# Performance work log

Measured on AMD Instinct MI355X. Metric: run time of the kernel, lower is better.

The kernel has to match this reference:

```python
import jax, jax.numpy as jnp
import numpy as np

B, S = 64, 200
DK = 32           # d_k = d_a = d_e
NQ = 4096         # n_question
NE = 20000        # n_exercise
NAT = 2000
NIT = 2000


def _xavier(k, shape):
    a = float(np.sqrt(6.0 / (shape[0] + shape[1])))
    return jax.random.uniform(k, shape, jnp.float32, -a, a)


def setup_inputs() -> dict:
    key = jax.random.key(0)
    ks = jax.random.split(key, 24)
    d = {}
    d['e_data'] = jax.random.randint(ks[0], (B, S), 0, NE)
    d['at_data'] = jax.random.randint(ks[1], (B, S), 0, NAT)
    d['it_data'] = jax.random.randint(ks[2], (B, S), 0, NIT)
    d['a_data'] = jax.random.randint(ks[3], (B, S), 0, 2).astype(jnp.float32)
    # binary Q-matrix: ~64 skills per exercise on average
    d['q_matrix'] = (jax.random.uniform(ks[4], (NE + 10, NQ + 1)) < (64.0 / NQ)).astype(jnp.float32)
    d['E_e'] = _xavier(ks[5], (NE + 10, DK))
    d['E_at'] = _xavier(ks[6], (NAT + 10, DK))
    d['E_it'] = _xavier(ks[7], (NIT + 10, DK))
    d['W1'] = _xavier(ks[8], (DK, 3 * DK)); d['b1'] = jnp.zeros((DK,), jnp.float32)
    d['W2'] = _xavier(ks[9], (DK, 4 * DK)); d['b2'] = jnp.zeros((DK,), jnp.float32)
    d['W3'] = _xavier(ks[10], (DK, 4 * DK)); d['b3'] = jnp.zeros((DK,), jnp.float32)
    d['W4'] = _xavier(ks[11], (DK, 3 * DK)); d['b4'] = jnp.zeros((DK,), jnp.float32)
    d['W5'] = _xavier(ks[12], (DK, 2 * DK)); d['b5'] = jnp.zeros((DK,), jnp.float32)
    d['h0'] = _xavier(ks[13], (NQ + 1, DK))
    return d


def _forward(e_data, at_data, it_data, a_data, q_matrix, E_e, E_at, E_it,
             W1, b1, W2, b2, W3, b3, W4, b4, W5, b5, h0):
    e_emb = E_e[e_data]                    # [B,S,DK]
    at_emb = E_at[at_data]                 # [B,S,DK]
    it_emb = E_it[it_data]                 # [B,S,DK]
    a_rep = jnp.broadcast_to(a_data[:, :, None], (B, S, DK))  # repeat answer to d_a
    all_learning = jnp.einsum('bsf,kf->bsk', jnp.concatenate([e_emb, at_emb, a_rep], -1), W1) + b1

    h_pre0 = jnp.broadcast_to(h0[None], (B, NQ + 1, DK))
    h_tilde0 = jnp.einsum('bn,bnd->bd', q_matrix[e_data[:, 0]], h_pre0)
    W4h, W4l, W4i = W4[:, :DK], W4[:, DK:2 * DK], W4[:, 2 * DK:]

    def step(carry, xs):
        learning_pre, h_pre, h_tilde_pre = carry
        e_t, it, learning, e_next_emb, e_next = xs
        q_e = q_matrix[e_t]                               # [B,NQ+1] gather
        x = jnp.concatenate([learning_pre, it, learning, h_tilde_pre], -1)  # [B,4DK]
        lg = jnp.tanh(x @ W2.T + b2)
        gl = jax.nn.sigmoid(x @ W3.T + b3)
        LG = gl * (lg + 1.0) * 0.5                        # [B,DK]
        LG_tilde = q_e[:, :, None] * LG[:, None, :]       # scatter (outer product), dropout off (eval)
        gamma_f = jax.nn.sigmoid(h_pre @ W4h.T + (LG @ W4l.T + it @ W4i.T + b4)[:, None, :])
        h = LG_tilde + gamma_f * h_pre                    # [B,NQ+1,DK]
        h_tilde = jnp.einsum('bn,bnd->bd', q_matrix[e_next], h)
        y = jax.nn.sigmoid(jnp.concatenate([e_next_emb, h_tilde], -1) @ W5.T + b5).sum(-1) / DK
        return (learning, h, h_tilde), y

    xs = (e_data[:, :-1].T,
          jnp.swapaxes(it_emb[:, :-1], 0, 1),
          jnp.swapaxes(all_learning[:, :-1], 0, 1),
          jnp.swapaxes(e_emb[:, 1:], 0, 1),
          e_data[:, 1:].T)
    init = (jnp.zeros((B, DK), jnp.float32), h_pre0, h_tilde0)
    _, ys = jax.lax.scan(step, init, xs)                  # ys: [S-1,B]
    pred = jnp.concatenate([jnp.zeros((B, 1), jnp.float32), ys.T], axis=1)
    return pred


def reference(e_data, at_data, it_data, a_data, q_matrix, E_e, E_at, E_it,
              W1, b1, W2, b2, W3, b3, W4, b4, W5, b5, h0):
    return _forward(e_data, at_data, it_data, a_data, q_matrix, E_e, E_at, E_it,
                    W1, b1, W2, b2, W3, b3, W4, b4, W5, b5, h0)
```

## Files before the change

### kernel.cpp

```cpp
#include <hip/hip_runtime.h>

#define Bv    64
#define Sv    200
#define DKv   32
#define NQ1v  4097
#define NWG   8
#define TPB   256
#define ROWS  2
#define NSTEP 199

typedef unsigned long long u64;

__device__ __forceinline__ float fsig(float x) {
  return __builtin_amdgcn_rcpf(1.0f + __builtin_amdgcn_exp2f(x * -1.4426950408889634f));
}
__device__ __forceinline__ float ftanh_(float x) {
  return fmaf(2.0f, fsig(2.0f * x), -1.0f);
}
__device__ __forceinline__ u64 packvt(float v, unsigned tag) {
  return ((u64)tag << 32) | (u64)__float_as_uint(v);
}
__device__ __forceinline__ u64 fresh_read(u64* p) {
  return __hip_atomic_fetch_add(p, 0ull, __ATOMIC_RELAXED, __HIP_MEMORY_SCOPE_AGENT);
}
__device__ __forceinline__ void fresh_write(u64* p, u64 v) {
  (void)__hip_atomic_exchange(p, v, __ATOMIC_RELAXED, __HIP_MEMORY_SCOPE_AGENT);
}

__global__ void lpkt_init(float* out) {
  int i = threadIdx.x;
  if (i < Bv) out[i * Sv] = 0.0f;
}

__global__ __launch_bounds__(TPB, 2) void lpkt_main(
    const int* __restrict__ e_data, const int* __restrict__ at_data,
    const int* __restrict__ it_data, const float* __restrict__ a_data,
    const float* __restrict__ q_matrix,
    const float* __restrict__ E_e, const float* __restrict__ E_at, const float* __restrict__ E_it,
    const float* __restrict__ W1, const float* __restrict__ b1,
    const float* __restrict__ W2, const float* __restrict__ b2,
    const float* __restrict__ W3, const float* __restrict__ b3,
    const float* __restrict__ W4, const float* __restrict__ b4,
    const float* __restrict__ W5, const float* __restrict__ b5,
    const float* __restrict__ h0, float* __restrict__ out,
    u64* __restrict__ partial)
{
  const int tid = threadIdx.x;
  const int wg  = blockIdx.x & (NWG - 1);
  const int b   = blockIdx.x / NWG;
  const int k   = tid & 31;
  const int p   = tid >> 5;
  const int nbase = wg * (TPB * ROWS);

  __shared__ float W23T[128 * 64];
  __shared__ __align__(16) float W1L[32 * 100];
  __shared__ __align__(16) float W4L[32 * 100];
  __shared__ __align__(16) float W5L[32 * 68];
  __shared__ float bL[5 * 32];
  __shared__ __align__(16) float xw_lds[96];
  __shared__ __align__(16) float it_lds[DKv];
  __shared__ __align__(16) float lcA[DKv], lcB[DKv];
  __shared__ __align__(16) float ht_lds[DKv];
  __shared__ __align__(16) float LG_lds[DKv];
  __shared__ __align__(16) float c_lds[DKv];
  __shared__ __align__(16) float red[8][DKv];
  __shared__ __align__(16) float red2[8][DKv];
  __shared__ float ht_part[DKv];
  __shared__ __align__(16) float h49[DKv];

  for (int idx = tid; idx < 128 * 32; idx += TPB) {
    int j = idx & 127, kk = idx >> 7;
    W23T[j * 64 + 2 * kk]     = W2[kk * 128 + j];
    W23T[j * 64 + 2 * kk + 1] = W3[kk * 128 + j];
  }
  for (int idx = tid; idx < 32 * 96; idx += TPB) {
    int r = idx / 96, c = idx % 96;
    W1L[r * 100 + c] = W1[idx];
    W4L[r * 100 + c] = W4[idx];
  }
  for (int idx = tid; idx < 32 * 64; idx += TPB) {
    int r = idx >> 6, c = idx & 63;
    W5L[r * 68 + c] = W5[idx];
  }
  if (tid < 32) {
    bL[0 * 32 + tid] = b1[tid]; bL[1 * 32 + tid] = b2[tid];
    bL[2 * 32 + tid] = b3[tid]; bL[3 * 32 + tid] = b4[tid];
    bL[4 * 32 + tid] = b5[tid];
  }
  if (tid < DKv) { ht_part[tid] = 0.0f; lcB[tid] = 0.0f; }
  if (wg == 0 && tid < DKv) h49[tid] = h0[4096 * DKv + tid];

  float h[ROWS][DKv];
#pragma unroll
  for (int r = 0; r < ROWS; r++) {
    const float4* hp = (const float4*)(h0 + (size_t)(nbase + r * TPB + tid) * DKv);
#pragma unroll
    for (int i = 0; i < 8; i++) {
      float4 v = hp[i];
      h[r][4*i] = v.x; h[r][4*i+1] = v.y; h[r][4*i+2] = v.z; h[r][4*i+3] = v.w;
    }
  }
  const int e0 = e_data[b * Sv];
  const float* q0 = q_matrix + (size_t)e0 * NQ1v;
  float qc[ROWS];
#pragma unroll
  for (int r = 0; r < ROWS; r++) qc[r] = q0[nbase + r * TPB + tid];
  float qc49 = (wg == 0 && tid < DKv) ? q0[4096] : 0.0f;
  __syncthreads();

#pragma unroll
  for (int r = 0; r < ROWS; r++) {
    if (qc[r] != 0.0f) {
#pragma unroll
      for (int kk = 0; kk < DKv; kk++) atomicAdd(&ht_part[kk], h[r][kk]);
    }
  }
  if (wg == 0 && tid < DKv && qc49 != 0.0f) atomicAdd(&ht_part[tid], h49[tid]);
  __syncthreads();
  if (tid < DKv)
    fresh_write(&partial[((size_t)(1 % 3) * Bv + b) * (NWG * DKv) + wg * DKv + tid],
                packvt(ht_part[tid], 1u));

  for (int t = 0; t < NSTEP; t++) {
    float* lc_cur  = (t & 1) ? lcB : lcA;
    float* lc_prev = (t & 1) ? lcA : lcB;
    const unsigned tau_g = (unsigned)(t + 1);
    const unsigned tau_p = (unsigned)(t + 2);

    const int ecur  = e_data[b * Sv + t];
    const int enext = e_data[b * Sv + t + 1];
    const int atc   = at_data[b * Sv + t];
    const int itc   = it_data[b * Sv + t];
    const float av  = a_data[b * Sv + t];
    const float* qnr = q_matrix + (size_t)enext * NQ1v;
    float qn[ROWS];
#pragma unroll
    for (int r = 0; r < ROWS; r++) qn[r] = qnr[nbase + r * TPB + tid];
    float qn49 = (wg == 0 && tid < DKv) ? qnr[4096] : 0.0f;

    if (tid < 96)
      xw_lds[tid] = (tid < 32) ? E_e[(size_t)ecur * DKv + tid]
                  : (tid < 64) ? E_at[(size_t)atc * DKv + (tid - 32)] : av;
    else if (tid < 128)
      it_lds[tid - 96] = E_it[(size_t)itc * DKv + (tid - 96)];

    float acc[ROWS][DKv];
#pragma unroll
    for (int kk = 0; kk < DKv; kk++) {
      float a0 = 0.0f, a1 = 0.0f;
#pragma unroll
      for (int d = 0; d < DKv; d += 4) {
        float4 w = *(const float4*)&W4[kk * 96 + d];
        a0 = fmaf(w.x, h[0][d+0], a0); a1 = fmaf(w.x, h[1][d+0], a1);
        a0 = fmaf(w.y, h[0][d+1], a0); a1 = fmaf(w.y, h[1][d+1], a1);
        a0 = fmaf(w.z, h[0][d+2], a0); a1 = fmaf(w.z, h[1][d+2], a1);
        a0 = fmaf(w.w, h[0][d+3], a0); a1 = fmaf(w.w, h[1][d+3], a1);
      }
      acc[0][kk] = a0; acc[1][kk] = a1;
    }
    __syncthreads();

    if (tid < DKv) {
      u64* pb = partial + ((size_t)(tau_g % 3) * Bv + b) * (NWG * DKv) + tid;
      u64 v[NWG];
      for (;;) {
        bool ok = true;
#pragma unroll
        for (int w2 = 0; w2 < NWG; w2++) {
          v[w2] = fresh_read(&pb[w2 * DKv]);
          ok = ok && ((unsigned)(v[w2] >> 32) == tau_g);
        }
        if (ok) break;
        __builtin_amdgcn_s_sleep(2);
      }
      float s = 0.0f;
#pragma unroll
      for (int w2 = 0; w2 < NWG; w2++) s += __uint_as_float((unsigned)v[w2]);
      ht_lds[tid] = s;
    } else if (tid >= 64 && tid < 96) {
      const int kx = tid - 64;
      float s = bL[0 * 32 + kx];
      const float4* wp = (const float4*)&W1L[kx * 100];
      const float4* xp = (const float4*)xw_lds;
#pragma unroll
      for (int i = 0; i < 24; i++) {
        float4 w = wp[i]; float4 x = xp[i];
        s = fmaf(x.x, w.x, s); s = fmaf(x.y, w.y, s);
        s = fmaf(x.z, w.z, s); s = fmaf(x.w, w.w, s);
      }
      lc_cur[kx] = s;
    }
    __syncthreads();

    {
      const int seg = p >> 1;
      const float* sp = (seg == 0) ? lc_prev : (seg == 1) ? it_lds
                      : (seg == 2) ? lc_cur  : ht_lds;
      const int off = (p & 1) * 16;
      float xv[16];
#pragma unroll
      for (int i = 0; i < 4; i++) {
        float4 v = ((const float4*)(sp + off))[i];
        xv[4*i] = v.x; xv[4*i+1] = v.y; xv[4*i+2] = v.z; xv[4*i+3] = v.w;
      }
      float s2 = 0.0f, s3 = 0.0f;
      const int jb = 16 * p;
#pragma unroll
      for (int i = 0; i < 16; i++) {
        float2 w = *(const float2*)&W23T[(jb + i) * 64 + 2 * k];
        s2 = fmaf(xv[i], w.x, s2);
        s3 = fmaf(xv[i], w.y, s3);
      }
      red[p][k] = s2; red2[p][k] = s3;
    }
    __syncthreads();

    if (tid < DKv) {
      float s2 = bL[1 * 32 + tid], s3 = bL[2 * 32 + tid];
#pragma unroll
      for (int pp = 0; pp < 8; pp++) { s2 += red[pp][tid]; s3 += red2[pp][tid]; }
      LG_lds[tid] = fsig(s3) * (ftanh_(s2) + 1.0f) * 0.5f;
    } else if (tid >= 128 && tid < 160) ht_part[tid - 128] = 0.0f;
    __syncthreads();

    {
      const float* up = (p < 4) ? (LG_lds + 8 * p) : (it_lds + 8 * (p - 4));
      const float4* wp = (const float4*)&W4L[k * 100 + 32 + 8 * p];
      float4 w0 = wp[0], w1 = wp[1];
      float pc = 0.0f;
      pc = fmaf(up[0], w0.x, pc); pc = fmaf(up[1], w0.y, pc);
      pc = fmaf(up[2], w0.z, pc); pc = fmaf(up[3], w0.w, pc);
      pc = fmaf(up[4], w1.x, pc); pc = fmaf(up[5], w1.y, pc);
      pc = fmaf(up[6], w1.z, pc); pc = fmaf(up[7], w1.w, pc);
      red[p][k] = pc;
    }
    if (wg == 0 && t >= 1 && tid >= 64 && tid < 128) {
      const int p2 = p - 2;
      const float* zs = (p2 == 0) ? xw_lds : ht_lds;
      const float4* wp = (const float4*)&W5L[k * 68 + 32 * p2];
      float acc5 = 0.0f;
#pragma unroll
      for (int i = 0; i < 8; i++) {
        float4 w = wp[i]; float4 z = ((const float4*)zs)[i];
        acc5 = fmaf(z.x, w.x, acc5); acc5 = fmaf(z.y, w.y, acc5);
        acc5 = fmaf(z.z, w.z, acc5); acc5 = fmaf(z.w, w.w, acc5);
      }
      red2[p2][k] = acc5;
    }
    __syncthreads();

    if (tid < DKv) {
      float s = bL[3 * 32 + tid];
#pragma unroll
      for (int pp = 0; pp < 8; pp++) s += red[pp][tid];
      c_lds[tid] = s;
    } else if (wg == 0 && t >= 1 && tid >= 96 && tid < 128) {
      const int kx = tid - 96;
      float s = fsig(bL[4 * 32 + kx] + red2[0][kx] + red2[1][kx]);
#pragma unroll
      for (int m = 1; m < 32; m <<= 1) s += __shfl_xor(s, m);
      if (tid == 96) out[b * Sv + t] = s * (1.0f / DKv);
    }
    __syncthreads();

    {
      float c_r[DKv], lg_r[DKv];
#pragma unroll
      for (int i = 0; i < 8; i++) {
        float4 cv = ((const float4*)c_lds)[i];
        float4 gv = ((const float4*)LG_lds)[i];
        c_r[4*i] = cv.x; c_r[4*i+1] = cv.y; c_r[4*i+2] = cv.z; c_r[4*i+3] = cv.w;
        lg_r[4*i] = gv.x; lg_r[4*i+1] = gv.y; lg_r[4*i+2] = gv.z; lg_r[4*i+3] = gv.w;
      }
#pragma unroll
      for (int r = 0; r < ROWS; r++) {
        const float qcr = qc[r];
#pragma unroll
        for (int kk = 0; kk < DKv; kk++) {
          float g = fsig(acc[r][kk] + c_r[kk]);
          h[r][kk] = fmaf(g, h[r][kk], qcr * lg_r[kk]);
        }
        if (qn[r] != 0.0f) {
#pragma unroll
          for (int kk = 0; kk < DKv; kk++) atomicAdd(&ht_part[kk], h[r][kk]);
        }
        qc[r] = qn[r];
      }
    }
    if (wg == 0 && tid < DKv) {
      float hh[DKv];
#pragma unroll
      for (int i = 0; i < 8; i++) {
        float4 v = ((const float4*)h49)[i];
        hh[4*i] = v.x; hh[4*i+1] = v.y; hh[4*i+2] = v.z; hh[4*i+3] = v.w;
      }
      float a = c_lds[tid];
#pragma unroll
      for (int d = 0; d < DKv; d += 4) {
        float4 w = *(const float4*)&W4L[tid * 100 + d];
        a = fmaf(w.x, hh[d+0], a); a = fmaf(w.y, hh[d+1], a);
        a = fmaf(w.z, hh[d+2], a); a = fmaf(w.w, hh[d+3], a);
      }
      float hn = fmaf(fsig(a), h49[tid], qc49 * LG_lds[tid]);
      h49[tid] = hn;
      if (qn49 != 0.0f) atomicAdd(&ht_part[tid], hn);
      qc49 = qn49;
    }
    __syncthreads();

    if (tid < DKv)
      fresh_write(&partial[((size_t)(tau_p % 3) * Bv + b) * (NWG * DKv) + wg * DKv + tid],
                  packvt(ht_part[tid], tau_p));
  }

  if (wg == 0) {
    const unsigned tau_f = (unsigned)(NSTEP + 1);
    if (tid < DKv) {
      u64* pb = partial + ((size_t)(tau_f % 3) * Bv + b) * (NWG * DKv) + tid;
      u64 v[NWG];
      for (;;) {
        bool ok = true;
#pragma unroll
        for (int w2 = 0; w2 < NWG; w2++) {
          v[w2] = fresh_read(&pb[w2 * DKv]);
          ok = ok && ((unsigned)(v[w2] >> 32) == tau_f);
        }
        if (ok) break;
        __builtin_amdgcn_s_sleep(2);
      }
      float s = 0.0f;
#pragma unroll
      for (int w2 = 0; w2 < NWG; w2++) s += __uint_as_float((unsigned)v[w2]);
      ht_lds[tid] = s;
      xw_lds[tid] = E_e[(size_t)e_data[b * Sv + 199] * DKv + tid];
    }
    __syncthreads();
    if (tid >= 64 && tid < 128) {
      const int p2 = p - 2;
      const float* zs = (p2 == 0) ? xw_lds : ht_lds;
      const float4* wp = (const float4*)&W5L[k * 68 + 32 * p2];
      float acc5 = 0.0f;
#pragma unroll
      for (int i = 0; i < 8; i++) {
        float4 w = wp[i]; float4 z = ((const float4*)zs)[i];
        acc5 = fmaf(z.x, w.x, acc5); acc5 = fmaf(z.y, w.y, acc5);
        acc5 = fmaf(z.z, w.z, acc5); acc5 = fmaf(z.w, w.w, acc5);
      }
      red2[p2][k] = acc5;
    }
    __syncthreads();
    if (tid >= 96 && tid < 128) {
      const int kx = tid - 96;
      float s = fsig(bL[4 * 32 + kx] + red2[0][kx] + red2[1][kx]);
#pragma unroll
      for (int m = 1; m < 32; m <<= 1) s += __shfl_xor(s, m);
      if (tid == 96) out[b * Sv + 199] = s * (1.0f / DKv);
    }
  }
}

extern "C" void kernel_launch(void* const* d_in, const int* in_sizes, int n_in,
                              void* d_out, int out_size, void* d_ws, size_t ws_size,
                              hipStream_t stream) {
  const int*   e_data   = (const int*)d_in[0];
  const int*   at_data  = (const int*)d_in[1];
  const int*   it_data  = (const int*)d_in[2];
  const float* a_data   = (const float*)d_in[3];
  const float* q_matrix = (const float*)d_in[4];
  const float* E_e      = (const float*)d_in[5];
  const float* E_at     = (const float*)d_in[6];
  const float* E_it     = (const float*)d_in[7];
  const float* W1 = (const float*)d_in[8];
  const float* b1 = (const float*)d_in[9];
  const float* W2 = (const float*)d_in[10];
  const float* b2 = (const float*)d_in[11];
  const float* W3 = (const float*)d_in[12];
  const float* b3 = (const float*)d_in[13];
  const float* W4 = (const float*)d_in[14];
  const float* b4 = (const float*)d_in[15];
  const float* W5 = (const float*)d_in[16];
  const float* b5 = (const float*)d_in[17];
  const float* h0 = (const float*)d_in[18];
  float* out = (float*)d_out;

  u64* partial = (u64*)d_ws;

  lpkt_init<<<1, 64, 0, stream>>>(out);
  lpkt_main<<<dim3(Bv * NWG), dim3(TPB), 0, stream>>>(
      e_data, at_data, it_data, a_data, q_matrix, E_e, E_at, E_it,
      W1, b1, W2, b2, W3, b3, W4, b4, W5, b5, h0, out, partial);
}
```

Baseline: 4.910 ms.

## Dedicate one master wave to the serial gate chain, workers compute row matvecs

Splits each workgroup into a 64-thread master wave and worker waves. The master polls the cross-workgroup partial sums and runs the whole W1/W2/W3/W4/W5 chain inside one wave, using LDS and lane shuffles instead of block barriers. Meanwhile the worker waves compute their rows' W4h·h products in parallel with it. The aim is to cut the per-step barrier count from about six to two and hide the small matvec chain behind the row work. The cost is that the master wave updates its own two rows after the barrier, which adds serial work at the end of each step, and the per-thread row assignment is rebalanced to match.

```diff
diff --git a/kernel.cpp b/kernel.cpp
--- a/kernel.cpp
+++ b/kernel.cpp
@@ -6,7 +6,6 @@
 #define NQ1v  4097
 #define NWG   8
 #define TPB   256
-#define ROWS  2
 #define NSTEP 199
 
 typedef unsigned long long u64;
@@ -48,314 +47,339 @@
   const int tid = threadIdx.x;
   const int wg  = blockIdx.x & (NWG - 1);
   const int b   = blockIdx.x / NWG;
-  const int k   = tid & 31;
-  const int p   = tid >> 5;
-  const int nbase = wg * (TPB * ROWS);
-
-  __shared__ float W23T[128 * 64];
-  __shared__ __align__(16) float W1L[32 * 100];
-  __shared__ __align__(16) float W4L[32 * 100];
-  __shared__ __align__(16) float W5L[32 * 68];
+  const int nbase = wg * 512;
+  const bool master = (tid < 64);
+
+  __shared__ float W1T[96 * 32];
+  __shared__ float W2T[128 * 32];
+  __shared__ float W3T[128 * 32];
+  __shared__ float W4T[96 * 32];
+  __shared__ float W5T[64 * 32];
   __shared__ float bL[5 * 32];
-  __shared__ __align__(16) float xw_lds[96];
-  __shared__ __align__(16) float it_lds[DKv];
-  __shared__ __align__(16) float lcA[DKv], lcB[DKv];
-  __shared__ __align__(16) float ht_lds[DKv];
+  __shared__ __align__(16) float xw[96];
+  __shared__ __align__(16) float xfull[128];
   __shared__ __align__(16) float LG_lds[DKv];
   __shared__ __align__(16) float c_lds[DKv];
-  __shared__ __align__(16) float red[8][DKv];
-  __shared__ __align__(16) float red2[8][DKv];
-  __shared__ float ht_part[DKv];
+  __shared__ __align__(16) float ht_part[DKv];
   __shared__ __align__(16) float h49[DKv];
 
-  for (int idx = tid; idx < 128 * 32; idx += TPB) {
-    int j = idx & 127, kk = idx >> 7;
-    W23T[j * 64 + 2 * kk]     = W2[kk * 128 + j];
-    W23T[j * 64 + 2 * kk + 1] = W3[kk * 128 + j];
-  }
   for (int idx = tid; idx < 32 * 96; idx += TPB) {
-    int r = idx / 96, c = idx % 96;
-    W1L[r * 100 + c] = W1[idx];
-    W4L[r * 100 + c] = W4[idx];
+    int kk = idx / 96, f = idx - kk * 96;
+    W1T[f * 32 + kk] = W1[idx];
+    W4T[f * 32 + kk] = W4[idx];
+  }
+  for (int idx = tid; idx < 32 * 128; idx += TPB) {
+    int kk = idx >> 7, f = idx & 127;
+    W2T[f * 32 + kk] = W2[idx];
+    W3T[f * 32 + kk] = W3[idx];
   }
   for (int idx = tid; idx < 32 * 64; idx += TPB) {
-    int r = idx >> 6, c = idx & 63;
-    W5L[r * 68 + c] = W5[idx];
+    int kk = idx >> 6, i = idx & 63;
+    W5T[i * 32 + kk] = W5[idx];
   }
   if (tid < 32) {
-    bL[0 * 32 + tid] = b1[tid]; bL[1 * 32 + tid] = b2[tid];
-    bL[2 * 32 + tid] = b3[tid]; bL[3 * 32 + tid] = b4[tid];
-    bL[4 * 32 + tid] = b5[tid];
-  }
-  if (tid < DKv) { ht_part[tid] = 0.0f; lcB[tid] = 0.0f; }
-  if (wg == 0 && tid < DKv) h49[tid] = h0[4096 * DKv + tid];
-
-  float h[ROWS][DKv];
-#pragma unroll
-  for (int r = 0; r < ROWS; r++) {
-    const float4* hp = (const float4*)(h0 + (size_t)(nbase + r * TPB + tid) * DKv);
+    bL[tid]       = b1[tid]; bL[32 + tid]  = b2[tid]; bL[64 + tid] = b3[tid];
+    bL[96 + tid]  = b4[tid]; bL[128 + tid] = b5[tid];
+    ht_part[tid] = 0.0f;
+  }
+  if (wg == 0 && tid < 32) h49[tid] = h0[(size_t)4096 * DKv + tid];
+
+  int row0, row1;
+  if (master) { row0 = nbase + 384 + tid;      row1 = nbase + 448 + tid; }
+  else        { int wt = tid - 64; row0 = nbase + wt; row1 = nbase + 192 + wt; }
+
+  float h[2][DKv];
+  {
+    const float4* hp0 = (const float4*)(h0 + (size_t)row0 * DKv);
+    const float4* hp1 = (const float4*)(h0 + (size_t)row1 * DKv);
 #pragma unroll
     for (int i = 0; i < 8; i++) {
-      float4 v = hp[i];
-      h[r][4*i] = v.x; h[r][4*i+1] = v.y; h[r][4*i+2] = v.z; h[r][4*i+3] = v.w;
+      float4 v0 = hp0[i], v1 = hp1[i];
+      h[0][4*i]=v0.x; h[0][4*i+1]=v0.y; h[0][4*i+2]=v0.z; h[0][4*i+3]=v0.w;
+      h[1][4*i]=v1.x; h[1][4*i+1]=v1.y; h[1][4*i+2]=v1.z; h[1][4*i+3]=v1.w;
     }
   }
   const int e0 = e_data[b * Sv];
   const float* q0 = q_matrix + (size_t)e0 * NQ1v;
-  float qc[ROWS];
-#pragma unroll
-  for (int r = 0; r < ROWS; r++) qc[r] = q0[nbase + r * TPB + tid];
-  float qc49 = (wg == 0 && tid < DKv) ? q0[4096] : 0.0f;
+  float qcv[2];
+  qcv[0] = q0[row0]; qcv[1] = q0[row1];
+  float qc49 = (wg == 0) ? q0[4096] : 0.0f;
   __syncthreads();
 
 #pragma unroll
-  for (int r = 0; r < ROWS; r++) {
-    if (qc[r] != 0.0f) {
+  for (int r = 0; r < 2; r++) {
+    if (qcv[r] != 0.0f) {
 #pragma unroll
       for (int kk = 0; kk < DKv; kk++) atomicAdd(&ht_part[kk], h[r][kk]);
     }
   }
-  if (wg == 0 && tid < DKv && qc49 != 0.0f) atomicAdd(&ht_part[tid], h49[tid]);
+  if (wg == 0 && tid < 32 && qc49 != 0.0f) atomicAdd(&ht_part[tid], h49[tid]);
   __syncthreads();
-  if (tid < DKv)
-    fresh_write(&partial[((size_t)(1 % 3) * Bv + b) * (NWG * DKv) + wg * DKv + tid],
+  if (tid < 32)
+    fresh_write(&partial[((size_t)1 * Bv + b) * (NWG * DKv) + wg * DKv + tid],
                 packvt(ht_part[tid], 1u));
 
+  float lp_reg = 0.0f;
+
   for (int t = 0; t < NSTEP; t++) {
-    float* lc_cur  = (t & 1) ? lcB : lcA;
-    float* lc_prev = (t & 1) ? lcA : lcB;
     const unsigned tau_g = (unsigned)(t + 1);
     const unsigned tau_p = (unsigned)(t + 2);
-
-    const int ecur  = e_data[b * Sv + t];
-    const int enext = e_data[b * Sv + t + 1];
-    const int atc   = at_data[b * Sv + t];
-    const int itc   = it_data[b * Sv + t];
-    const float av  = a_data[b * Sv + t];
-    const float* qnr = q_matrix + (size_t)enext * NQ1v;
-    float qn[ROWS];
-#pragma unroll
-    for (int r = 0; r < ROWS; r++) qn[r] = qnr[nbase + r * TPB + tid];
-    float qn49 = (wg == 0 && tid < DKv) ? qnr[4096] : 0.0f;
-
-    if (tid < 96)
-      xw_lds[tid] = (tid < 32) ? E_e[(size_t)ecur * DKv + tid]
-                  : (tid < 64) ? E_at[(size_t)atc * DKv + (tid - 32)] : av;
-    else if (tid < 128)
-      it_lds[tid - 96] = E_it[(size_t)itc * DKv + (tid - 96)];
-
-    float acc[ROWS][DKv];
-#pragma unroll
-    for (int kk = 0; kk < DKv; kk++) {
-      float a0 = 0.0f, a1 = 0.0f;
-#pragma unroll
-      for (int d = 0; d < DKv; d += 4) {
-        float4 w = *(const float4*)&W4[kk * 96 + d];
-        a0 = fmaf(w.x, h[0][d+0], a0); a1 = fmaf(w.x, h[1][d+0], a1);
-        a0 = fmaf(w.y, h[0][d+1], a0); a1 = fmaf(w.y, h[1][d+1], a1);
-        a0 = fmaf(w.z, h[0][d+2], a0); a1 = fmaf(w.z, h[1][d+2], a1);
-        a0 = fmaf(w.w, h[0][d+3], a0); a1 = fmaf(w.w, h[1][d+3], a1);
-      }
-      acc[0][kk] = a0; acc[1][kk] = a1;
-    }
-    __syncthreads();
-
-    if (tid < DKv) {
-      u64* pb = partial + ((size_t)(tau_g % 3) * Bv + b) * (NWG * DKv) + tid;
-      u64 v[NWG];
+    float acc[2][DKv];
+    float qnv[2];
+    float qn49 = 0.0f;
+
+    if (master) {
+      const int j = tid & 31, hf = tid >> 5;
+      const int ecur  = e_data[b * Sv + t];
+      const int enext = e_data[b * Sv + t + 1];
+      const int atc   = at_data[b * Sv + t];
+      const int itc   = it_data[b * Sv + t];
+      const float av  = a_data[b * Sv + t];
+      const float ee  = E_e[(size_t)ecur * DKv + j];
+      const float ea  = E_at[(size_t)atc * DKv + j];
+      const float ei  = E_it[(size_t)itc * DKv + j];
+      const float* qnr = q_matrix + (size_t)enext * NQ1v;
+      qnv[0] = qnr[row0]; qnv[1] = qnr[row1];
+      if (wg == 0) qn49 = qnr[4096];
+
+      u64* pb = partial + ((size_t)(tau_g % 3) * Bv + b) * (NWG * DKv) + j;
+      u64 v[4];
       for (;;) {
         bool ok = true;
 #pragma unroll
-        for (int w2 = 0; w2 < NWG; w2++) {
-          v[w2] = fresh_read(&pb[w2 * DKv]);
-          ok = ok && ((unsigned)(v[w2] >> 32) == tau_g);
-        }
-        if (ok) break;
+        for (int c = 0; c < 4; c++) {
+          v[c] = fresh_read(&pb[(hf + 2 * c) * DKv]);
+          ok = ok && ((unsigned)(v[c] >> 32) == tau_g);
+        }
+        if (__all(ok)) break;
         __builtin_amdgcn_s_sleep(2);
       }
-      float s = 0.0f;
-#pragma unroll
-      for (int w2 = 0; w2 < NWG; w2++) s += __uint_as_float((unsigned)v[w2]);
-      ht_lds[tid] = s;
-    } else if (tid >= 64 && tid < 96) {
-      const int kx = tid - 64;
-      float s = bL[0 * 32 + kx];
-      const float4* wp = (const float4*)&W1L[kx * 100];
-      const float4* xp = (const float4*)xw_lds;
-#pragma unroll
-      for (int i = 0; i < 24; i++) {
-        float4 w = wp[i]; float4 x = xp[i];
-        s = fmaf(x.x, w.x, s); s = fmaf(x.y, w.y, s);
-        s = fmaf(x.z, w.z, s); s = fmaf(x.w, w.w, s);
-      }
-      lc_cur[kx] = s;
+      float hs = 0.0f;
+#pragma unroll
+      for (int c = 0; c < 4; c++) hs += __uint_as_float((unsigned)v[c]);
+      hs += __shfl_xor(hs, 32);
+      const float htv = hs;
+
+      if (tid < 32) ht_part[tid] = 0.0f;
+
+      if (tid < 32) { xw[tid] = ee; xw[64 + tid] = av;
+                      xfull[tid] = lp_reg; xfull[96 + tid] = htv; }
+      else          { xw[tid] = ea; xfull[tid] = ei; }
+
+      float s1 = 0.0f;
+      {
+        const float4* xp = (const float4*)(xw + 48 * hf);
+#pragma unroll
+        for (int i = 0; i < 12; i++) {
+          float4 x4 = xp[i];
+          const float* wv = &W1T[(48 * hf + 4 * i) * 32 + j];
+          s1 = fmaf(x4.x, wv[0],  s1);
+          s1 = fmaf(x4.y, wv[32], s1);
+          s1 = fmaf(x4.z, wv[64], s1);
+          s1 = fmaf(x4.w, wv[96], s1);
+        }
+      }
+      s1 += __shfl_xor(s1, 32);
+      const float lc = s1 + bL[j];
+      if (tid < 32) xfull[64 + tid] = lc;
+
+      float s2 = 0.0f, s3 = 0.0f;
+      {
+        const float4* xp = (const float4*)(xfull + 64 * hf);
+#pragma unroll
+        for (int i = 0; i < 16; i++) {
+          float4 x4 = xp[i];
+          const int f = (64 * hf + 4 * i) * 32 + j;
+          const float* w2 = &W2T[f];
+          const float* w3 = &W3T[f];
+          s2 = fmaf(x4.x, w2[0],  s2); s3 = fmaf(x4.x, w3[0],  s3);
+          s2 = fmaf(x4.y, w2[32], s2); s3 = fmaf(x4.y, w3[32], s3);
+          s2 = fmaf(x4.z, w2[64], s2); s3 = fmaf(x4.z, w3[64], s3);
+          s2 = fmaf(x4.w, w2[96], s2); s3 = fmaf(x4.w, w3[96], s3);
+        }
+      }
+      s2 += __shfl_xor(s2, 32);
+      s3 += __shfl_xor(s3, 32);
+      const float LGv = fsig(s3 + bL[64 + j]) * (ftanh_(s2 + bL[32 + j]) + 1.0f) * 0.5f;
+      if (tid < 32) LG_lds[tid] = LGv;
+
+      float sc = 0.0f;
+      {
+        const float4* up = (const float4*)(hf ? (xfull + 32) : LG_lds);
+#pragma unroll
+        for (int i = 0; i < 8; i++) {
+          float4 u4 = up[i];
+          const float* wv = &W4T[(32 + 32 * hf + 4 * i) * 32 + j];
+          sc = fmaf(u4.x, wv[0],  sc);
+          sc = fmaf(u4.y, wv[32], sc);
+          sc = fmaf(u4.z, wv[64], sc);
+          sc = fmaf(u4.w, wv[96], sc);
+        }
+      }
+      sc += __shfl_xor(sc, 32);
+      const float cv = sc + bL[96 + j];
+      if (tid < 32) c_lds[tid] = cv;
+
+      if (wg == 0 && t >= 1) {
+        float s5 = 0.0f;
+        const float4* zp = (const float4*)(hf ? (xfull + 96) : xw);
+#pragma unroll
+        for (int i = 0; i < 8; i++) {
+          float4 z4 = zp[i];
+          const float* wv = &W5T[(32 * hf + 4 * i) * 32 + j];
+          s5 = fmaf(z4.x, wv[0],  s5);
+          s5 = fmaf(z4.y, wv[32], s5);
+          s5 = fmaf(z4.z, wv[64], s5);
+          s5 = fmaf(z4.w, wv[96], s5);
+        }
+        s5 += __shfl_xor(s5, 32);
+        float yv = fsig(s5 + bL[128 + j]);
+#pragma unroll
+        for (int m = 1; m < 32; m <<= 1) yv += __shfl_xor(yv, m);
+        if (tid == 0) out[b * Sv + t] = yv * (1.0f / DKv);
+      }
+      lp_reg = lc;
+    } else {
+      const int enext = e_data[b * Sv + t + 1];
+      const float* qnr = q_matrix + (size_t)enext * NQ1v;
+      qnv[0] = qnr[row0]; qnv[1] = qnr[row1];
+#pragma unroll
+      for (int kk = 0; kk < DKv; kk++) {
+        float a0 = 0.0f, a1 = 0.0f;
+#pragma unroll
+        for (int d = 0; d < DKv; d += 4) {
+          float4 w = *(const float4*)&W4[kk * 96 + d];
+          a0 = fmaf(w.x, h[0][d+0], a0); a1 = fmaf(w.x, h[1][d+0], a1);
+          a0 = fmaf(w.y, h[0][d+1], a0); a1 = fmaf(w.y, h[1][d+1], a1);
+          a0 = fmaf(w.z, h[0][d+2], a0); a1 = fmaf(w.z, h[1][d+2], a1);
+          a0 = fmaf(w.w, h[0][d+3], a0); a1 = fmaf(w.w, h[1][d+3], a1);
+        }
+        acc[0][kk] = a0; acc[1][kk] = a1;
+      }
     }
     __syncthreads();
 
-    {
-      const int seg = p >> 1;
-      const float* sp = (seg == 0) ? lc_prev : (seg == 1) ? it_lds
-                      : (seg == 2) ? lc_cur  : ht_lds;
-      const int off = (p & 1) * 16;
-      float xv[16];
-#pragma unroll
-      for (int i = 0; i < 4; i++) {
-        float4 v = ((const float4*)(sp + off))[i];
-        xv[4*i] = v.x; xv[4*i+1] = v.y; xv[4*i+2] = v.z; xv[4*i+3] = v.w;
-      }
-      float s2 = 0.0f, s3 = 0.0f;
-      const int jb = 16 * p;
-#pragma unroll
-      for (int i = 0; i < 16; i++) {
-        float2 w = *(const float2*)&W23T[(jb + i) * 64 + 2 * k];
-        s2 = fmaf(xv[i], w.x, s2);
-        s3 = fmaf(xv[i], w.y, s3);
-      }
-      red[p][k] = s2; red2[p][k] = s3;
-    }
-    __syncthreads();
-
-    if (tid < DKv) {
-      float s2 = bL[1 * 32 + tid], s3 = bL[2 * 32 + tid];
-#pragma unroll
-      for (int pp = 0; pp < 8; pp++) { s2 += red[pp][tid]; s3 += red2[pp][tid]; }
-      LG_lds[tid] = fsig(s3) * (ftanh_(s2) + 1.0f) * 0.5f;
-    } else if (tid >= 128 && tid < 160) ht_part[tid - 128] = 0.0f;
-    __syncthreads();
-
-    {
-      const float* up = (p < 4) ? (LG_lds + 8 * p) : (it_lds + 8 * (p - 4));
-      const float4* wp = (const float4*)&W4L[k * 100 + 32 + 8 * p];
-      float4 w0 = wp[0], w1 = wp[1];
-      float pc = 0.0f;
-      pc = fmaf(up[0], w0.x, pc); pc = fmaf(up[1], w0.y, pc);
-      pc = fmaf(up[2], w0.z, pc); pc = fmaf(up[3], w0.w, pc);
-      pc = fmaf(up[4], w1.x, pc); pc = fmaf(up[5], w1.y, pc);
-      pc = fmaf(up[6], w1.z, pc); pc = fmaf(up[7], w1.w, pc);
-      red[p][k] = pc;
-    }
-    if (wg == 0 && t >= 1 && tid >= 64 && tid < 128) {
-      const int p2 = p - 2;
-      const float* zs = (p2 == 0) ? xw_lds : ht_lds;
-      const float4* wp = (const float4*)&W5L[k * 68 + 32 * p2];
-      float acc5 = 0.0f;
+    if (!master) {
+      float c_r[DKv], lg_r[DKv];
 #pragma unroll
       for (int i = 0; i < 8; i++) {
-        float4 w = wp[i]; float4 z = ((const float4*)zs)[i];
-        acc5 = fmaf(z.x, w.x, acc5); acc5 = fmaf(z.y, w.y, acc5);
-        acc5 = fmaf(z.z, w.z, acc5); acc5 = fmaf(z.w, w.w, acc5);
-      }
-      red2[p2][k] = acc5;
-    }
-    __syncthreads();
-
-    if (tid < DKv) {
-      float s = bL[3 * 32 + tid];
-#pragma unroll
-      for (int pp = 0; pp < 8; pp++) s += red[pp][tid];
-      c_lds[tid] = s;
-    } else if (wg == 0 && t >= 1 && tid >= 96 && tid < 128) {
-      const int kx = tid - 96;
-      float s = fsig(bL[4 * 32 + kx] + red2[0][kx] + red2[1][kx]);
-#pragma unroll
-      for (int m = 1; m < 32; m <<= 1) s += __shfl_xor(s, m);
-      if (tid == 96) out[b * Sv + t] = s * (1.0f / DKv);
-    }
-    __syncthreads();
-
-    {
-      float c_r[DKv], lg_r[DKv];
-#pragma unroll
-      for (int i = 0; i < 8; i++) {
-        float4 cv = ((const float4*)c_lds)[i];
-        float4 gv = ((const float4*)LG_lds)[i];
-        c_r[4*i] = cv.x; c_r[4*i+1] = cv.y; c_r[4*i+2] = cv.z; c_r[4*i+3] = cv.w;
-        lg_r[4*i] = gv.x; lg_r[4*i+1] = gv.y; lg_r[4*i+2] = gv.z; lg_r[4*i+3] = gv.w;
-      }
-#pragma unroll
-      for (int r = 0; r < ROWS; r++) {
-        const float qcr = qc[r];
+        float4 cc = ((const float4*)c_lds)[i];
+        float4 gg = ((const float4*)LG_lds)[i];
+        c_r[4*i]=cc.x; c_r[4*i+1]=cc.y; c_r[4*i+2]=cc.z; c_r[4*i+3]=cc.w;
+        lg_r[4*i]=gg.x; lg_r[4*i+1]=gg.y; lg_r[4*i+2]=gg.z; lg_r[4*i+3]=gg.w;
+      }
+#pragma unroll
+      for (int r = 0; r < 2; r++) {
+        const float qcr = qcv[r];
 #pragma unroll
         for (int kk = 0; kk < DKv; kk++) {
           float g = fsig(acc[r][kk] + c_r[kk]);
           h[r][kk] = fmaf(g, h[r][kk], qcr * lg_r[kk]);
         }
-        if (qn[r] != 0.0f) {
+        if (qnv[r] != 0.0f) {
 #pragma unroll
           for (int kk = 0; kk < DKv; kk++) atomicAdd(&ht_part[kk], h[r][kk]);
         }
-        qc[r] = qn[r];
-      }
-    }
-    if (wg == 0 && tid < DKv) {
-      float hh[DKv];
+        qcv[r] = qnv[r];
+      }
+    }
+    __syncthreads();
+
+    if (master) {
+#pragma unroll
+      for (int kk = 0; kk < DKv; kk++) {
+        float a0 = 0.0f, a1 = 0.0f;
+#pragma unroll
+        for (int d = 0; d < DKv; d += 4) {
+          float4 w = *(const float4*)&W4[kk * 96 + d];
+          a0 = fmaf(w.x, h[0][d+0], a0); a1 = fmaf(w.x, h[1][d+0], a1);
+          a0 = fmaf(w.y, h[0][d+1], a0); a1 = fmaf(w.y, h[1][d+1], a1);
+          a0 = fmaf(w.z, h[0][d+2], a0); a1 = fmaf(w.z, h[1][d+2], a1);
+          a0 = fmaf(w.w, h[0][d+3], a0); a1 = fmaf(w.w, h[1][d+3], a1);
+        }
+        acc[0][kk] = a0; acc[1][kk] = a1;
+      }
+      float c_r[DKv], lg_r[DKv];
 #pragma unroll
       for (int i = 0; i < 8; i++) {
-        float4 v = ((const float4*)h49)[i];
-        hh[4*i] = v.x; hh[4*i+1] = v.y; hh[4*i+2] = v.z; hh[4*i+3] = v.w;
-      }
-      float a = c_lds[tid];
-#pragma unroll
-      for (int d = 0; d < DKv; d += 4) {
-        float4 w = *(const float4*)&W4L[tid * 100 + d];
-        a = fmaf(w.x, hh[d+0], a); a = fmaf(w.y, hh[d+1], a);
-        a = fmaf(w.z, hh[d+2], a); a = fmaf(w.w, hh[d+3], a);
-      }
-      float hn = fmaf(fsig(a), h49[tid], qc49 * LG_lds[tid]);
-      h49[tid] = hn;
-      if (qn49 != 0.0f) atomicAdd(&ht_part[tid], hn);
+        float4 cc = ((const float4*)c_lds)[i];
+        float4 gg = ((const float4*)LG_lds)[i];
+        c_r[4*i]=cc.x; c_r[4*i+1]=cc.y; c_r[4*i+2]=cc.z; c_r[4*i+3]=cc.w;
+        lg_r[4*i]=gg.x; lg_r[4*i+1]=gg.y; lg_r[4*i+2]=gg.z; lg_r[4*i+3]=gg.w;
+      }
+#pragma unroll
+      for (int r = 0; r < 2; r++) {
+        const float qcr = qcv[r];
+#pragma unroll
+        for (int kk = 0; kk < DKv; kk++) {
+          float g = fsig(acc[r][kk] + c_r[kk]);
+          h[r][kk] = fmaf(g, h[r][kk], qcr * lg_r[kk]);
+        }
+        if (qnv[r] != 0.0f) {
+#pragma unroll
+          for (int kk = 0; kk < DKv; kk++) atomicAdd(&ht_part[kk], h[r][kk]);
+        }
+        qcv[r] = qnv[r];
+      }
+      if (wg == 0 && tid < 32) {
+        float a49 = c_r[tid & 31] * 0.0f + c_lds[tid];
+#pragma unroll
+        for (int d = 0; d < 32; d += 4) {
+          float4 hv = *(const float4*)&h49[d];
+          a49 = fmaf(hv.x, W4T[(d+0)*32 + tid], a49);
+          a49 = fmaf(hv.y, W4T[(d+1)*32 + tid], a49);
+          a49 = fmaf(hv.z, W4T[(d+2)*32 + tid], a49);
+          a49 = fmaf(hv.w, W4T[(d+3)*32 + tid], a49);
+        }
+        float hn = fmaf(fsig(a49), h49[tid], qc49 * LG_lds[tid]);
+        h49[tid] = hn;
+        if (qn49 != 0.0f) atomicAdd(&ht_part[tid], hn);
+      }
       qc49 = qn49;
-    }
-    __syncthreads();
-
-    if (tid < DKv)
-      fresh_write(&partial[((size_t)(tau_p % 3) * Bv + b) * (NWG * DKv) + wg * DKv + tid],
-                  packvt(ht_part[tid], tau_p));
-  }
-
-  if (wg == 0) {
+      if (tid < 32)
+        fresh_write(&partial[((size_t)(tau_p % 3) * Bv + b) * (NWG * DKv) + wg * DKv + tid],
+                    packvt(ht_part[tid], tau_p));
+    }
+  }
+
+  if (wg == 0 && master) {
+    const int j = tid & 31, hf = tid >> 5;
     const unsigned tau_f = (unsigned)(NSTEP + 1);
-    if (tid < DKv) {
-      u64* pb = partial + ((size_t)(tau_f % 3) * Bv + b) * (NWG * DKv) + tid;
-      u64 v[NWG];
-      for (;;) {
-        bool ok = true;
-#pragma unroll
-        for (int w2 = 0; w2 < NWG; w2++) {
-          v[w2] = fresh_read(&pb[w2 * DKv]);
-          ok = ok && ((unsigned)(v[w2] >> 32) == tau_f);
-        }
-        if (ok) break;
-        __builtin_amdgcn_s_sleep(2);
-      }
-      float s = 0.0f;
-#pragma unroll
-      for (int w2 = 0; w2 < NWG; w2++) s += __uint_as_float((unsigned)v[w2]);
-      ht_lds[tid] = s;
-      xw_lds[tid] = E_e[(size_t)e_data[b * Sv + 199] * DKv + tid];
-    }
-    __syncthreads();
-    if (tid >= 64 && tid < 128) {
-      const int p2 = p - 2;
-      const float* zs = (p2 == 0) ? xw_lds : ht_lds;
-      const float4* wp = (const float4*)&W5L[k * 68 + 32 * p2];
-      float acc5 = 0.0f;
-#pragma unroll
-      for (int i = 0; i < 8; i++) {
-        float4 w = wp[i]; float4 z = ((const float4*)zs)[i];
-        acc5 = fmaf(z.x, w.x, acc5); acc5 = fmaf(z.y, w.y, acc5);
-        acc5 = fmaf(z.z, w.z, acc5); acc5 = fmaf(z.w, w.w, acc5);
-      }
-      red2[p2][k] = acc5;
-    }
-    __syncthreads();
-    if (tid >= 96 && tid < 128) {
-      const int kx = tid - 96;
-      float s = fsig(bL[4 * 32 + kx] + red2[0][kx] + red2[1][kx]);
-#pragma unroll
-      for (int m = 1; m < 32; m <<= 1) s += __shfl_xor(s, m);
-      if (tid == 96) out[b * Sv + 199] = s * (1.0f / DKv);
-    }
+    u64* pb = partial + ((size_t)(tau_f % 3) * Bv + b) * (NWG * DKv) + j;
+    u64 v[4];
+    for (;;) {
+      bool ok = true;
+#pragma unroll
+      for (int c = 0; c < 4; c++) {
+        v[c] = fresh_read(&pb[(hf + 2 * c) * DKv]);
+        ok = ok && ((unsigned)(v[c] >> 32) == tau_f);
+      }
+      if (__all(ok)) break;
+      __builtin_amdgcn_s_sleep(2);
+    }
+    float hs = 0.0f;
+#pragma unroll
+    for (int c = 0; c < 4; c++) hs += __uint_as_float((unsigned)v[c]);
+    hs += __shfl_xor(hs, 32);
+    const int e199 = e_data[b * Sv + 199];
+    const float ee = E_e[(size_t)e199 * DKv + j];
+    if (tid < 32) { xw[tid] = ee; xfull[96 + tid] = hs; }
+    float s5 = 0.0f;
+    const float4* zp = (const float4*)(hf ? (xfull + 96) : xw);
+#pragma unroll
+    for (int i = 0; i < 8; i++) {
+      float4 z4 = zp[i];
+      const float* wv = &W5T[(32 * hf + 4 * i) * 32 + j];
+      s5 = fmaf(z4.x, wv[0],  s5);
+      s5 = fmaf(z4.y, wv[32], s5);
+      s5 = fmaf(z4.z, wv[64], s5);
+      s5 = fmaf(z4.w, wv[96], s5);
+    }
+    s5 += __shfl_xor(s5, 32);
+    float yv = fsig(s5 + bL[128 + j]);
+#pragma unroll
+    for (int m = 1; m < 32; m <<= 1) yv += __shfl_xor(yv, m);
+    if (tid == 0) out[b * Sv + 199] = yv * (1.0f / DKv);
   }
 }
 
```

Measured after the change: 7.110 ms. 44.8% more time.

## Add volatile mailbox fast-path for cross-workgroup partial sum exchange

Applied to the files above, without the earlier changes.

Each workgroup now writes its per-step partial h_tilde to a second mailbox buffer with a plain volatile store, alongside the atomic write. Waiting workgroups first poll that mailbox with plain volatile loads for a bounded number of tries, then fall back to the atomic fresh-read spin loop. The block-to-batch mapping also changes so that the eight workgroups of one batch are spread across the grid rather than adjacent, which changes XCD and L2 placement. Volatile loads may hit a non-coherent cache, so the fast path could spin uselessly or add latency, and it adds extra stores each step.

```diff
diff --git a/kernel.cpp b/kernel.cpp
--- a/kernel.cpp
+++ b/kernel.cpp
@@ -8,6 +8,7 @@
 #define TPB   256
 #define ROWS  2
 #define NSTEP 199
+#define FASTN 16
 
 typedef unsigned long long u64;
 
@@ -43,11 +44,11 @@
     const float* __restrict__ W4, const float* __restrict__ b4,
     const float* __restrict__ W5, const float* __restrict__ b5,
     const float* __restrict__ h0, float* __restrict__ out,
-    u64* __restrict__ partial)
+    u64* __restrict__ partial, u64* __restrict__ mailbox)
 {
   const int tid = threadIdx.x;
-  const int wg  = blockIdx.x & (NWG - 1);
-  const int b   = blockIdx.x / NWG;
+  const int b   = blockIdx.x & 63;
+  const int wg  = blockIdx.x >> 6;
   const int k   = tid & 31;
   const int p   = tid >> 5;
   const int nbase = wg * (TPB * ROWS);
@@ -117,9 +118,12 @@
   }
   if (wg == 0 && tid < DKv && qc49 != 0.0f) atomicAdd(&ht_part[tid], h49[tid]);
   __syncthreads();
-  if (tid < DKv)
-    fresh_write(&partial[((size_t)(1 % 3) * Bv + b) * (NWG * DKv) + wg * DKv + tid],
-                packvt(ht_part[tid], 1u));
+  if (tid < DKv) {
+    const u64 pv = packvt(ht_part[tid], 1u);
+    volatile u64* mb = mailbox + ((size_t)(1 % 3) * Bv + b) * (NWG * DKv) + wg * DKv + tid;
+    *mb = pv;
+    fresh_write(&partial[((size_t)(1 % 3) * Bv + b) * (NWG * DKv) + wg * DKv + tid], pv);
+  }
 
   for (int t = 0; t < NSTEP; t++) {
     float* lc_cur  = (t & 1) ? lcB : lcA;
@@ -161,17 +165,33 @@
     __syncthreads();
 
     if (tid < DKv) {
-      u64* pb = partial + ((size_t)(tau_g % 3) * Bv + b) * (NWG * DKv) + tid;
       u64 v[NWG];
-      for (;;) {
-        bool ok = true;
-#pragma unroll
-        for (int w2 = 0; w2 < NWG; w2++) {
-          v[w2] = fresh_read(&pb[w2 * DKv]);
-          ok = ok && ((unsigned)(v[w2] >> 32) == tau_g);
-        }
-        if (ok) break;
-        __builtin_amdgcn_s_sleep(2);
+      bool ok = false;
+      {
+        const volatile u64* mb =
+            mailbox + ((size_t)(tau_g % 3) * Bv + b) * (NWG * DKv) + tid;
+        for (int it = 0; it < FASTN && !ok; ++it) {
+          ok = true;
+#pragma unroll
+          for (int w2 = 0; w2 < NWG; w2++) {
+            v[w2] = mb[w2 * DKv];
+            ok = ok && ((unsigned)(v[w2] >> 32) == tau_g);
+          }
+          if (!ok) __builtin_amdgcn_s_sleep(1);
+        }
+      }
+      if (!ok) {
+        u64* pb = partial + ((size_t)(tau_g % 3) * Bv + b) * (NWG * DKv) + tid;
+        for (;;) {
+          ok = true;
+#pragma unroll
+          for (int w2 = 0; w2 < NWG; w2++) {
+            v[w2] = fresh_read(&pb[w2 * DKv]);
+            ok = ok && ((unsigned)(v[w2] >> 32) == tau_g);
+          }
+          if (ok) break;
+          __builtin_amdgcn_s_sleep(2);
+        }
       }
       float s = 0.0f;
 #pragma unroll
@@ -308,25 +328,46 @@
     }
     __syncthreads();
 
-    if (tid < DKv)
+    if (tid < DKv) {
+      const u64 pv = packvt(ht_part[tid], tau_p);
+      volatile u64* mb =
+          mailbox + ((size_t)(tau_p % 3) * Bv + b) * (NWG * DKv) + wg * DKv + tid;
+      *mb = pv;
       fresh_write(&partial[((size_t)(tau_p % 3) * Bv + b) * (NWG * DKv) + wg * DKv + tid],
-                  packvt(ht_part[tid], tau_p));
+                  pv);
+    }
   }
 
   if (wg == 0) {
     const unsigned tau_f = (unsigned)(NSTEP + 1);
     if (tid < DKv) {
-      u64* pb = partial + ((size_t)(tau_f % 3) * Bv + b) * (NWG * DKv) + tid;
       u64 v[NWG];
-      for (;;) {
-        bool ok = true;
-#pragma unroll
-        for (int w2 = 0; w2 < NWG; w2++) {
-          v[w2] = fresh_read(&pb[w2 * DKv]);
-          ok = ok && ((unsigned)(v[w2] >> 32) == tau_f);
-        }
-        if (ok) break;
-        __builtin_amdgcn_s_sleep(2);
+      bool ok = false;
+      {
+        const volatile u64* mb =
+            mailbox + ((size_t)(tau_f % 3) * Bv + b) * (NWG * DKv) + tid;
+        for (int it = 0; it < FASTN && !ok; ++it) {
+          ok = true;
+#pragma unroll
+          for (int w2 = 0; w2 < NWG; w2++) {
+            v[w2] = mb[w2 * DKv];
+            ok = ok && ((unsigned)(v[w2] >> 32) == tau_f);
+          }
+          if (!ok) __builtin_amdgcn_s_sleep(1);
+        }
+      }
+      if (!ok) {
+        u64* pb = partial + ((size_t)(tau_f % 3) * Bv + b) * (NWG * DKv) + tid;
+        for (;;) {
+          ok = true;
+#pragma unroll
+          for (int w2 = 0; w2 < NWG; w2++) {
+            v[w2] = fresh_read(&pb[w2 * DKv]);
+            ok = ok && ((unsigned)(v[w2] >> 32) == tau_f);
+          }
+          if (ok) break;
+          __builtin_amdgcn_s_sleep(2);
+        }
       }
       float s = 0.0f;
 #pragma unroll
@@ -384,9 +425,10 @@
   float* out = (float*)d_out;
 
   u64* partial = (u64*)d_ws;
+  u64* mailbox = partial + (size_t)3 * Bv * NWG * DKv;
 
   lpkt_init<<<1, 64, 0, stream>>>(out);
   lpkt_main<<<dim3(Bv * NWG), dim3(TPB), 0, stream>>>(
       e_data, at_data, it_data, a_data, q_matrix, E_e, E_at, E_it,
-      W1, b1, W2, b2, W3, b3, W4, b4, W5, b5, h0, out, partial);
-}
+      W1, b1, W2, b2, W3, b3, W4, b4, W5, b5, h0, out, partial, mailbox);
+}
```

Result: slower. 5.416 ms (+10.3%).
